# Performance work log

Measured on AMD Instinct MI355X. Metric: run time of the kernel, lower is better.

The kernel has to match this reference:

```python
import jax, jax.numpy as jnp
import numpy as np

ROPE_BASE = 10000.0

def _rope_tables(pos, d_head):
    # pos: (T,) int; returns cos,sin of shape (T, d_head//2)
    half = d_head // 2
    inv_freq = 1.0 / (ROPE_BASE ** (jnp.arange(half, dtype=jnp.float32) / half))
    ang = pos.astype(jnp.float32)[:, None] * inv_freq[None, :]
    return jnp.cos(ang), jnp.sin(ang)

def _apply_rope(x, cos, sin):
    # x: (B, H, T, D); cos/sin: (T, D//2); rotate-half convention
    x1, x2 = jnp.split(x, 2, axis=-1)
    c = cos[None, None, :, :]
    s = sin[None, None, :, :]
    return jnp.concatenate([x1 * c - x2 * s, x1 * s + x2 * c], axis=-1)

def setup_inputs() -> dict:
    key = jax.random.key(0)
    ks = jax.random.split(key, 8)
    B, T, C = 16, 4, 2048
    n_head, n_kv_head, d_head = 16, 4, 128
    S_cache = 4096
    sd = 1.0 / np.sqrt(C)
    return {
        "x": jax.random.normal(ks[0], (B, T, C), dtype=jnp.float32),
        "cache_k": jax.random.normal(ks[1], (B, n_kv_head, S_cache, d_head), dtype=jnp.float32),
        "cache_v": jax.random.normal(ks[2], (B, n_kv_head, S_cache, d_head), dtype=jnp.float32),
        "wq": jax.random.normal(ks[3], (C, n_head * d_head), dtype=jnp.float32) * sd,
        "wk": jax.random.normal(ks[4], (C, n_kv_head * d_head), dtype=jnp.float32) * sd,
        "wv": jax.random.normal(ks[5], (C, n_kv_head * d_head), dtype=jnp.float32) * sd,
        "w_proj": jax.random.normal(ks[6], (C, C), dtype=jnp.float32) * sd,
        "start_pos": 4096,
    }

def reference(x, cache_k, cache_v, wq, wk, wv, w_proj, start_pos):
    B, T, C = x.shape
    n_head, n_kv_head = 16, 4
    d_head = C // n_head
    group_size = n_head // n_kv_head
    sliding_window, sink = 2048, 4

    # projections -> (B, H, T, D)
    q = (x @ wq).reshape(B, T, n_head, d_head).transpose(0, 2, 1, 3)
    k = (x @ wk).reshape(B, T, n_kv_head, d_head).transpose(0, 2, 1, 3)
    v = (x @ wv).reshape(B, T, n_kv_head, d_head).transpose(0, 2, 1, 3)

    # RoPE at absolute positions [start_pos, start_pos+T)
    pos = jnp.arange(start_pos, start_pos + T)
    cos, sin = _rope_tables(pos, d_head)
    q = _apply_rope(q, cos, sin)
    k = _apply_rope(k, cos, sin)

    # KV cache concat along sequence dim
    k_all = jnp.concatenate([cache_k, k], axis=2)
    v_all = jnp.concatenate([cache_v, v], axis=2)

    # sliding window + attention sink slicing (4096+T > 2048+4)
    if k_all.shape[2] > sliding_window + sink:
        k_all = jnp.concatenate([k_all[:, :, :sink, :], k_all[:, :, -sliding_window:, :]], axis=2)
        v_all = jnp.concatenate([v_all[:, :, :sink, :], v_all[:, :, -sliding_window:, :]], axis=2)

    # GQA: expand KV heads to match query heads (repeat_interleave on head dim)
    k_attn = jnp.repeat(k_all, group_size, axis=1)
    v_attn = jnp.repeat(v_all, group_size, axis=1)

    # SDPA, is_causal=False (decode path with cache), dropout=0 (eval)
    scale = 1.0 / jnp.sqrt(jnp.float32(d_head))
    scores = jnp.einsum('bhtd,bhsd->bhts', q, k_attn) * scale
    attn = jax.nn.softmax(scores, axis=-1)
    y = jnp.einsum('bhts,bhsd->bhtd', attn, v_attn)

    y = y.transpose(0, 2, 1, 3).reshape(B, T, C)
    return y @ w_proj
```

## Files before the change

### kernel.cpp

```cpp
#include <hip/hip_runtime.h>
#include <math.h>

#define BB   16
#define TT   4
#define CC   2048
#define NH   16
#define NKV  4
#define DH   128
#define GRP  4
#define SCACHE 4096
#define SATT 2052
#define CS   128
#define NCH  17
#define KSPL 8

typedef unsigned int  uint32;
typedef unsigned short ushort_t;
typedef __attribute__((ext_vector_type(8))) __bf16 bf16x8;
typedef __attribute__((ext_vector_type(4))) float  f32x4;

__device__ __forceinline__ uint32 f2bf_bits(float f) {
    uint32 u = __float_as_uint(f);
    return (u + 0x7FFFu + ((u >> 16) & 1u)) >> 16;
}
__device__ __forceinline__ uint32 pk2(float lo, float hi) {
    return f2bf_bits(lo) | (f2bf_bits(hi) << 16);
}

#define Q_OFF    0
#define KNEW_OFF 524288
#define VNEW_OFF 655360
#define Y_OFF    786432
#define SCR_OFF  1310720

__global__ __launch_bounds__(256) void k_qkv(
    const float* __restrict__ x, const float* __restrict__ wq,
    const float* __restrict__ wk, const float* __restrict__ wv,
    float* __restrict__ part_qkv)
{
    __shared__ float xs[64][256];
    int ns = blockIdx.x, ks = blockIdx.y;
    int tid = threadIdx.x;
    int k0 = ks * 256;

    #pragma unroll
    for (int it = 0; it < 16; ++it) {
        int slot = it * 256 + tid;
        int row = slot >> 6, c4 = slot & 63;
        *(float4*)&xs[row][c4 * 4] = *(const float4*)(x + (size_t)row * CC + k0 + c4 * 4);
    }
    __syncthreads();

    int cp = tid & 31, rg = tid >> 5;
    const float* wp; int ldw, col;
    if (ns < 32)      { ldw = 2048; col = ns * 64 + cp * 2;
                        wp = wq + (size_t)k0 * 2048 + ns * 64 + cp * 2; }
    else if (ns < 40) { ldw = 512;  col = 2048 + (ns - 32) * 64 + cp * 2;
                        wp = wk + (size_t)k0 * 512 + (ns - 32) * 64 + cp * 2; }
    else              { ldw = 512;  col = 2560 + (ns - 40) * 64 + cp * 2;
                        wp = wv + (size_t)k0 * 512 + (ns - 40) * 64 + cp * 2; }

    float a[16];
    #pragma unroll
    for (int i = 0; i < 16; ++i) a[i] = 0.f;

    for (int k = 0; k < 256; k += 4) {
        float2 w0 = *(const float2*)(wp);
        float2 w1 = *(const float2*)(wp + ldw);
        float2 w2 = *(const float2*)(wp + 2 * ldw);
        float2 w3 = *(const float2*)(wp + 3 * ldw);
        wp += 4 * ldw;
        #pragma unroll
        for (int m = 0; m < 8; ++m) {
            float4 xv = *(const float4*)&xs[rg * 8 + m][k];
            float s0 = a[2*m], s1 = a[2*m+1];
            s0 = fmaf(xv.x, w0.x, s0); s1 = fmaf(xv.x, w0.y, s1);
            s0 = fmaf(xv.y, w1.x, s0); s1 = fmaf(xv.y, w1.y, s1);
            s0 = fmaf(xv.z, w2.x, s0); s1 = fmaf(xv.z, w2.y, s1);
            s0 = fmaf(xv.w, w3.x, s0); s1 = fmaf(xv.w, w3.y, s1);
            a[2*m] = s0; a[2*m+1] = s1;
        }
    }
    #pragma unroll
    for (int m = 0; m < 8; ++m)
        *(float2*)(part_qkv + ((size_t)(ks * 64 + rg * 8 + m) * 3072) + col) =
            make_float2(a[2*m], a[2*m+1]);
}

__global__ __launch_bounds__(256) void k_fix(
    const float* __restrict__ part_qkv, const int* __restrict__ spp,
    float* __restrict__ qws, float* __restrict__ knew, float* __restrict__ vnew)
{
    int u = blockIdx.x * 256 + threadIdx.x;
    int m = blockIdx.y;
    int b = m >> 2, t = m & 3;
    int sp = spp[0];
    const float NEG_L2_10K_64 = -0.20762050593048633f;

    if (u < 1024) {
        int h = u >> 6, d = u & 63;
        int col = h * 128 + d;
        float s1 = 0.f, s2 = 0.f;
        #pragma unroll
        for (int ks = 0; ks < KSPL; ++ks) {
            const float* p = part_qkv + (size_t)(ks * 64 + m) * 3072;
            s1 += p[col]; s2 += p[col + 64];
        }
        float inv = exp2f((float)d * NEG_L2_10K_64);
        float ang = (float)(sp + t) * inv;
        float cc = cosf(ang), ss = sinf(ang);
        float* dst = qws + (size_t)((b * NH + h) * TT + t) * DH + d;
        dst[0]  = s1 * cc - s2 * ss;
        dst[64] = s1 * ss + s2 * cc;
    } else if (u < 1280) {
        int v = u - 1024;
        int kv = v >> 6, d = v & 63;
        int col = 2048 + kv * 128 + d;
        float s1 = 0.f, s2 = 0.f;
        #pragma unroll
        for (int ks = 0; ks < KSPL; ++ks) {
            const float* p = part_qkv + (size_t)(ks * 64 + m) * 3072;
            s1 += p[col]; s2 += p[col + 64];
        }
        float inv = exp2f((float)d * NEG_L2_10K_64);
        float ang = (float)(sp + t) * inv;
        float cc = cosf(ang), ss = sinf(ang);
        float* dst = knew + (size_t)((b * NKV + kv) * TT + t) * DH + d;
        dst[0]  = s1 * cc - s2 * ss;
        dst[64] = s1 * ss + s2 * cc;
    } else {
        int v = u - 1280;
        int c0 = v * 2;
        int kv = c0 >> 7, dd = c0 & 127;
        float s1 = 0.f, s2 = 0.f;
        #pragma unroll
        for (int ks = 0; ks < KSPL; ++ks) {
            const float* p = part_qkv + (size_t)(ks * 64 + m) * 3072 + 2560 + c0;
            s1 += p[0]; s2 += p[1];
        }
        float* dst = vnew + (size_t)((b * NKV + kv) * TT + t) * DH + dd;
        dst[0] = s1; dst[1] = s2;
    }
}

__device__ __forceinline__ const float* kv_row(
    const float* cache, const float* newt, int bk, int j)
{
    if (j < 4)         return cache + ((size_t)bk * SCACHE + j) * DH;
    else if (j < 2048) return cache + ((size_t)bk * SCACHE + j + 2048) * DH;
    else               return newt  + ((size_t)(bk * TT + (j - 2048))) * DH;
}

__global__ __launch_bounds__(256) void k_attn(
    const float* __restrict__ qws,
    const float* __restrict__ kc, const float* __restrict__ vc,
    const float* __restrict__ knew, const float* __restrict__ vnew,
    float* __restrict__ part)
{
    __shared__ ushort_t vt_lds[128 * 136];
    __shared__ ushort_t p_lds[16 * 136];
    __shared__ float    red_a[64];
    __shared__ float    red_b[64];

    int bx = blockIdx.x;
    int c  = bx % NCH;
    int bk = bx / NCH;
    int b  = bk >> 2, kvh = bk & 3;
    int j0 = c * CS;
    int jn = (SATT - j0 < CS) ? (SATT - j0) : CS;
    int tid  = threadIdx.x;
    int wave = tid >> 6, lane = tid & 63;
    int quad = lane >> 4, l15 = lane & 15;
    const float scale = 0.08838834764831845f;

    int n0 = wave * 32;

    int rA = n0 + l15, rB = n0 + 16 + l15;
    const float* kA = kv_row(kc, knew, bk, j0 + (rA < jn ? rA : 0));
    const float* kB = kv_row(kc, knew, bk, j0 + (rB < jn ? rB : 0));
    float4 ka[8], kb[8];
    #pragma unroll
    for (int ks = 0; ks < 4; ++ks) {
        const float* pa = kA + ks * 32 + quad * 8;
        const float* pb = kB + ks * 32 + quad * 8;
        ka[2*ks]   = *(const float4*)pa;
        ka[2*ks+1] = *(const float4*)(pa + 4);
        kb[2*ks]   = *(const float4*)pb;
        kb[2*ks+1] = *(const float4*)(pb + 4);
    }

    int key0 = 2 * lane;
    bool okA = key0 < jn, okB = key0 + 1 < jn;
    const float* rva = kv_row(vc, vnew, bk, j0 + (okA ? key0 : 0));
    const float* rvb = kv_row(vc, vnew, bk, j0 + (okB ? key0 + 1 : 0));
    float4 va0[4], vb0[4];
    #pragma unroll
    for (int i = 0; i < 4; ++i) {
        int d = n0 + i * 4;
        va0[i] = *(const float4*)(rva + d);
        vb0[i] = *(const float4*)(rvb + d);
    }

    bf16x8 aq[4];
    {
        int h = kvh * GRP + (l15 >> 2), t = l15 & 3;
        const float* qr = qws + (size_t)((b * NH + h) * TT + t) * DH;
        #pragma unroll
        for (int ks = 0; ks < 4; ++ks) {
            const float* s = qr + ks * 32 + quad * 8;
            float4 f0 = *(const float4*)s;
            float4 f1 = *(const float4*)(s + 4);
            union { uint32 u[4]; bf16x8 v; } pk;
            pk.u[0] = pk2(f0.x, f0.y); pk.u[1] = pk2(f0.z, f0.w);
            pk.u[2] = pk2(f1.x, f1.y); pk.u[3] = pk2(f1.z, f1.w);
            aq[ks] = pk.v;
        }
    }

    f32x4 s0 = {0.f, 0.f, 0.f, 0.f}, s1 = {0.f, 0.f, 0.f, 0.f};
    #pragma unroll
    for (int ks = 0; ks < 4; ++ks) {
        union { uint32 u[4]; bf16x8 v; } pa, pb;
        pa.u[0] = pk2(ka[2*ks].x,   ka[2*ks].y);
        pa.u[1] = pk2(ka[2*ks].z,   ka[2*ks].w);
        pa.u[2] = pk2(ka[2*ks+1].x, ka[2*ks+1].y);
        pa.u[3] = pk2(ka[2*ks+1].z, ka[2*ks+1].w);
        pb.u[0] = pk2(kb[2*ks].x,   kb[2*ks].y);
        pb.u[1] = pk2(kb[2*ks].z,   kb[2*ks].w);
        pb.u[2] = pk2(kb[2*ks+1].x, kb[2*ks+1].y);
        pb.u[3] = pk2(kb[2*ks+1].z, kb[2*ks+1].w);
        s0 = __builtin_amdgcn_mfma_f32_16x16x32_bf16(aq[ks], pa.v, s0, 0, 0, 0);
        s1 = __builtin_amdgcn_mfma_f32_16x16x32_bf16(aq[ks], pb.v, s1, 0, 0, 0);
    }

    uint32* vt32 = (uint32*)vt_lds;
    #pragma unroll
    for (int i = 0; i < 4; ++i) {
        int d = n0 + i * 4;
        float4 fa = okA ? va0[i] : make_float4(0.f, 0.f, 0.f, 0.f);
        float4 fb = okB ? vb0[i] : make_float4(0.f, 0.f, 0.f, 0.f);
        vt32[(d + 0) * 68 + lane] = pk2(fa.x, fb.x);
        vt32[(d + 1) * 68 + lane] = pk2(fa.y, fb.y);
        vt32[(d + 2) * 68 + lane] = pk2(fa.z, fb.z);
        vt32[(d + 3) * 68 + lane] = pk2(fa.w, fb.w);
    }
    float4 va1[4], vb1[4];
    #pragma unroll
    for (int i = 0; i < 4; ++i) {
        int d = n0 + 16 + i * 4;
        va1[i] = *(const float4*)(rva + d);
        vb1[i] = *(const float4*)(rvb + d);
    }

    int c0 = n0 + l15, c1 = n0 + 16 + l15;
    bool v0ok = c0 < jn, v1ok = c1 < jn;
    float sc0[4], sc1[4];
    #pragma unroll
    for (int i = 0; i < 4; ++i) {
        sc0[i] = v0ok ? s0[i] * scale : -1e30f;
        sc1[i] = v1ok ? s1[i] * scale : -1e30f;
        float v = fmaxf(sc0[i], sc1[i]);
        v = fmaxf(v, __shfl_xor(v, 1));
        v = fmaxf(v, __shfl_xor(v, 2));
        v = fmaxf(v, __shfl_xor(v, 4));
        v = fmaxf(v, __shfl_xor(v, 8));
        if (l15 == 0) red_a[wave * 16 + quad * 4 + i] = v;
    }
    __syncthreads();

    #pragma unroll
    for (int i = 0; i < 4; ++i) {
        int r = quad * 4 + i;
        float M = fmaxf(fmaxf(red_a[r], red_a[16 + r]),
                        fmaxf(red_a[32 + r], red_a[48 + r]));
        float p0 = __expf(sc0[i] - M);
        float p1 = __expf(sc1[i] - M);
        p_lds[r * 136 + c0] = (ushort_t)f2bf_bits(p0);
        p_lds[r * 136 + c1] = (ushort_t)f2bf_bits(p1);
        float v = p0 + p1;
        v += __shfl_xor(v, 1);
        v += __shfl_xor(v, 2);
        v += __shfl_xor(v, 4);
        v += __shfl_xor(v, 8);
        if (l15 == 0) red_b[wave * 16 + r] = v;
    }

    #pragma unroll
    for (int i = 0; i < 4; ++i) {
        int d = n0 + 16 + i * 4;
        float4 fa = okA ? va1[i] : make_float4(0.f, 0.f, 0.f, 0.f);
        float4 fb = okB ? vb1[i] : make_float4(0.f, 0.f, 0.f, 0.f);
        vt32[(d + 0) * 68 + lane] = pk2(fa.x, fb.x);
        vt32[(d + 1) * 68 + lane] = pk2(fa.y, fb.y);
        vt32[(d + 2) * 68 + lane] = pk2(fa.z, fb.z);
        vt32[(d + 3) * 68 + lane] = pk2(fa.w, fb.w);
    }
    __syncthreads();

    if (tid < 16) {
        int r = tid;
        float M = fmaxf(fmaxf(red_a[r], red_a[16 + r]),
                        fmaxf(red_a[32 + r], red_a[48 + r]));
        float L = red_b[r] + red_b[16 + r] + red_b[32 + r] + red_b[48 + r];
        float* rp = part + ((size_t)(bk * NCH + c) * 16 + r) * 132;
        rp[0] = M; rp[1] = L;
    }

    int d0 = wave * 32;
    f32x4 o0 = {0.f, 0.f, 0.f, 0.f}, o1 = {0.f, 0.f, 0.f, 0.f};
    #pragma unroll
    for (int ks = 0; ks < 4; ++ks) {
        bf16x8 ap = *(const bf16x8*)&p_lds[l15 * 136 + ks * 32 + quad * 8];
        bf16x8 b0 = *(const bf16x8*)&vt_lds[(d0 + l15) * 136 + ks * 32 + quad * 8];
        bf16x8 b1 = *(const bf16x8*)&vt_lds[(d0 + 16 + l15) * 136 + ks * 32 + quad * 8];
        o0 = __builtin_amdgcn_mfma_f32_16x16x32_bf16(ap, b0, o0, 0, 0, 0);
        o1 = __builtin_amdgcn_mfma_f32_16x16x32_bf16(ap, b1, o1, 0, 0, 0);
    }
    float* dstb = part + (size_t)(bk * NCH + c) * 16 * 132;
    #pragma unroll
    for (int i = 0; i < 4; ++i) {
        int row = quad * 4 + i;
        dstb[row * 132 + 4 + d0 + l15]      = o0[i];
        dstb[row * 132 + 4 + d0 + 16 + l15] = o1[i];
    }
}

__global__ __launch_bounds__(128) void k_comb(
    const float* __restrict__ part, float* __restrict__ yws)
{
    int bx = blockIdx.x;
    int t = bx & 3, h = (bx >> 2) & 15, b = bx >> 6;
    int bk = b * NKV + (h >> 2);
    int r  = (h & 3) * 4 + t;
    int d  = threadIdx.x;
    float M = -1e30f;
    for (int c = 0; c < NCH; ++c)
        M = fmaxf(M, part[((size_t)(bk * NCH + c) * 16 + r) * 132]);
    float L = 0.f, y = 0.f;
    for (int c = 0; c < NCH; ++c) {
        const float* pp = part + ((size_t)(bk * NCH + c) * 16 + r) * 132;
        float w = __expf(pp[0] - M);
        L += w * pp[1];
        y  = fmaf(w, pp[4 + d], y);
    }
    yws[(size_t)(b * TT + t) * CC + h * DH + d] = y / L;
}

__global__ __launch_bounds__(256) void k_proj(
    const float* __restrict__ yws, const float* __restrict__ wp,
    float* __restrict__ part_p)
{
    __shared__ float xs[64][256];
    int ns = blockIdx.x, ks = blockIdx.y;
    int tid = threadIdx.x;
    int k0 = ks * 256;
    #pragma unroll
    for (int it = 0; it < 16; ++it) {
        int slot = it * 256 + tid;
        int row = slot >> 6, c4 = slot & 63;
        *(float4*)&xs[row][c4 * 4] = *(const float4*)(yws + (size_t)row * CC + k0 + c4 * 4);
    }
    __syncthreads();

    int cp = tid & 31, rg = tid >> 5;
    int n = ns * 64 + cp * 2;
    const float* w = wp + (size_t)k0 * CC + n;
    float a[16];
    #pragma unroll
    for (int i = 0; i < 16; ++i) a[i] = 0.f;

    for (int k = 0; k < 256; k += 4) {
        float2 w0 = *(const float2*)(w);
        float2 w1 = *(const float2*)(w + CC);
        float2 w2 = *(const float2*)(w + 2 * CC);
        float2 w3 = *(const float2*)(w + 3 * CC);
        w += 4 * CC;
        #pragma unroll
        for (int m = 0; m < 8; ++m) {
            float4 xv = *(const float4*)&xs[rg * 8 + m][k];
            float s0 = a[2*m], s1 = a[2*m+1];
            s0 = fmaf(xv.x, w0.x, s0); s1 = fmaf(xv.x, w0.y, s1);
            s0 = fmaf(xv.y, w1.x, s0); s1 = fmaf(xv.y, w1.y, s1);
            s0 = fmaf(xv.z, w2.x, s0); s1 = fmaf(xv.z, w2.y, s1);
            s0 = fmaf(xv.w, w3.x, s0); s1 = fmaf(xv.w, w3.y, s1);
            a[2*m] = s0; a[2*m+1] = s1;
        }
    }
    #pragma unroll
    for (int m = 0; m < 8; ++m)
        *(float2*)(part_p + ((size_t)(ks * 64 + rg * 8 + m) * CC) + n) =
            make_float2(a[2*m], a[2*m+1]);
}

__global__ __launch_bounds__(256) void k_out(
    const float* __restrict__ part_p, float* __restrict__ out)
{
    int gt = blockIdx.x * 256 + threadIdx.x;
    float s = 0.f;
    #pragma unroll
    for (int ks = 0; ks < KSPL; ++ks) s += part_p[(size_t)ks * 64 * CC + gt];
    out[gt] = s;
}

extern "C" void kernel_launch(void* const* d_in, const int* in_sizes, int n_in,
                              void* d_out, int out_size, void* d_ws, size_t ws_size,
                              hipStream_t stream)
{
    const float* x   = (const float*)d_in[0];
    const float* ck  = (const float*)d_in[1];
    const float* cv  = (const float*)d_in[2];
    const float* wq  = (const float*)d_in[3];
    const float* wk  = (const float*)d_in[4];
    const float* wv  = (const float*)d_in[5];
    const float* wpj = (const float*)d_in[6];
    const int*   sp  = (const int*)d_in[7];
    char* ws = (char*)d_ws;
    float* qws  = (float*)(ws + Q_OFF);
    float* knew = (float*)(ws + KNEW_OFF);
    float* vnew = (float*)(ws + VNEW_OFF);
    float* yws  = (float*)(ws + Y_OFF);
    float* scr  = (float*)(ws + SCR_OFF);
    float* out  = (float*)d_out;

    hipLaunchKernelGGL(k_qkv,  dim3(48, 8),   dim3(256), 0, stream, x, wq, wk, wv, scr);
    hipLaunchKernelGGL(k_fix,  dim3(6, 64),   dim3(256), 0, stream, scr, sp, qws, knew, vnew);
    hipLaunchKernelGGL(k_attn, dim3(64 * NCH), dim3(256), 0, stream, qws, ck, cv, knew, vnew, scr);
    hipLaunchKernelGGL(k_comb, dim3(1024),    dim3(128), 0, stream, scr, yws);
    hipLaunchKernelGGL(k_proj, dim3(32, 8),   dim3(256), 0, stream, yws, wpj, scr);
    hipLaunchKernelGGL(k_out,  dim3(512),     dim3(256), 0, stream, scr, out);
}
```

Measured before the change: 369.0 us.

## Make attention chunk waves independent with per-wave softmax and cross-wave merge

Each wave now owns 32 keys: it computes a local max and exp, writes its own P and a transposed, XOR-swizzled bf16 V tile into private LDS, and runs the full P·V over all 128 head dims. The block-wide max barrier between QK and PV goes away. Partial outputs from the four waves are rescaled and summed through LDS at the end, and the softmax scale is folded into Q before the bf16 conversion. This trades an extra LDS reduction pass and more accumulator registers for less synchronisation and fewer bank conflicts.

```diff
diff --git a/kernel.cpp b/kernel.cpp
--- a/kernel.cpp
+++ b/kernel.cpp
@@ -26,6 +26,7 @@
 __device__ __forceinline__ uint32 pk2(float lo, float hi) {
     return f2bf_bits(lo) | (f2bf_bits(hi) << 16);
 }
+#define F4C(v, j) ((j)==0 ? (v).x : (j)==1 ? (v).y : (j)==2 ? (v).z : (v).w)
 
 #define Q_OFF    0
 #define KNEW_OFF 524288
@@ -157,10 +158,7 @@
     const float* __restrict__ knew, const float* __restrict__ vnew,
     float* __restrict__ part)
 {
-    __shared__ ushort_t vt_lds[128 * 136];
-    __shared__ ushort_t p_lds[16 * 136];
-    __shared__ float    red_a[64];
-    __shared__ float    red_b[64];
+    __shared__ __align__(16) uint32 smem[9600];
 
     int bx = blockIdx.x;
     int c  = bx % NCH;
@@ -169,36 +167,39 @@
     int j0 = c * CS;
     int jn = (SATT - j0 < CS) ? (SATT - j0) : CS;
     int tid  = threadIdx.x;
-    int wave = tid >> 6, lane = tid & 63;
+    int w    = tid >> 6, lane = tid & 63;
     int quad = lane >> 4, l15 = lane & 15;
     const float scale = 0.08838834764831845f;
 
-    int n0 = wave * 32;
-
-    int rA = n0 + l15, rB = n0 + 16 + l15;
-    const float* kA = kv_row(kc, knew, bk, j0 + (rA < jn ? rA : 0));
-    const float* kB = kv_row(kc, knew, bk, j0 + (rB < jn ? rB : 0));
+    uint32*   vt    = smem + w * 2048;
+    ushort_t* pl    = (ushort_t*)(smem + 8448) + w * 512;
+    float*    red_m = (float*)(smem + 9472);
+    float*    red_l = red_m + 64;
+    float*    o_all = (float*)smem;
+
+    int base = w * 32;
+
+    int rA = base + l15, rB = base + 16 + l15;
+    const float* kAp = kv_row(kc, knew, bk, j0 + (rA < jn ? rA : 0));
+    const float* kBp = kv_row(kc, knew, bk, j0 + (rB < jn ? rB : 0));
     float4 ka[8], kb[8];
     #pragma unroll
     for (int ks = 0; ks < 4; ++ks) {
-        const float* pa = kA + ks * 32 + quad * 8;
-        const float* pb = kB + ks * 32 + quad * 8;
-        ka[2*ks]   = *(const float4*)pa;
-        ka[2*ks+1] = *(const float4*)(pa + 4);
-        kb[2*ks]   = *(const float4*)pb;
-        kb[2*ks+1] = *(const float4*)(pb + 4);
-    }
-
-    int key0 = 2 * lane;
-    bool okA = key0 < jn, okB = key0 + 1 < jn;
+        ka[2*ks]   = *(const float4*)(kAp + ks * 32 + quad * 8);
+        ka[2*ks+1] = *(const float4*)(kAp + ks * 32 + quad * 8 + 4);
+        kb[2*ks]   = *(const float4*)(kBp + ks * 32 + quad * 8);
+        kb[2*ks+1] = *(const float4*)(kBp + ks * 32 + quad * 8 + 4);
+    }
+
+    int key0 = base + 2 * l15, key1 = key0 + 1;
+    bool okA = key0 < jn, okB = key1 < jn;
     const float* rva = kv_row(vc, vnew, bk, j0 + (okA ? key0 : 0));
-    const float* rvb = kv_row(vc, vnew, bk, j0 + (okB ? key0 + 1 : 0));
-    float4 va0[4], vb0[4];
-    #pragma unroll
-    for (int i = 0; i < 4; ++i) {
-        int d = n0 + i * 4;
-        va0[i] = *(const float4*)(rva + d);
-        vb0[i] = *(const float4*)(rvb + d);
+    const float* rvb = kv_row(vc, vnew, bk, j0 + (okB ? key1 : 0));
+    float4 va[4], vb[4];
+    #pragma unroll
+    for (int i = 0; i < 4; ++i) {
+        va[i] = *(const float4*)(rva + quad * 32 + i * 4);
+        vb[i] = *(const float4*)(rvb + quad * 32 + i * 4);
     }
 
     bf16x8 aq[4];
@@ -207,13 +208,14 @@
         const float* qr = qws + (size_t)((b * NH + h) * TT + t) * DH;
         #pragma unroll
         for (int ks = 0; ks < 4; ++ks) {
-            const float* s = qr + ks * 32 + quad * 8;
-            float4 f0 = *(const float4*)s;
-            float4 f1 = *(const float4*)(s + 4);
-            union { uint32 u[4]; bf16x8 v; } pk;
-            pk.u[0] = pk2(f0.x, f0.y); pk.u[1] = pk2(f0.z, f0.w);
-            pk.u[2] = pk2(f1.x, f1.y); pk.u[3] = pk2(f1.z, f1.w);
-            aq[ks] = pk.v;
+            float4 f0 = *(const float4*)(qr + ks * 32 + quad * 8);
+            float4 f1 = *(const float4*)(qr + ks * 32 + quad * 8 + 4);
+            union { uint32 u[4]; bf16x8 v; } pk_;
+            pk_.u[0] = pk2(f0.x * scale, f0.y * scale);
+            pk_.u[1] = pk2(f0.z * scale, f0.w * scale);
+            pk_.u[2] = pk2(f1.x * scale, f1.y * scale);
+            pk_.u[3] = pk2(f1.z * scale, f1.w * scale);
+            aq[ks] = pk_.v;
         }
     }
 
@@ -233,95 +235,113 @@
         s1 = __builtin_amdgcn_mfma_f32_16x16x32_bf16(aq[ks], pb.v, s1, 0, 0, 0);
     }
 
-    uint32* vt32 = (uint32*)vt_lds;
-    #pragma unroll
-    for (int i = 0; i < 4; ++i) {
-        int d = n0 + i * 4;
-        float4 fa = okA ? va0[i] : make_float4(0.f, 0.f, 0.f, 0.f);
-        float4 fb = okB ? vb0[i] : make_float4(0.f, 0.f, 0.f, 0.f);
-        vt32[(d + 0) * 68 + lane] = pk2(fa.x, fb.x);
-        vt32[(d + 1) * 68 + lane] = pk2(fa.y, fb.y);
-        vt32[(d + 2) * 68 + lane] = pk2(fa.z, fb.z);
-        vt32[(d + 3) * 68 + lane] = pk2(fa.w, fb.w);
-    }
-    float4 va1[4], vb1[4];
-    #pragma unroll
-    for (int i = 0; i < 4; ++i) {
-        int d = n0 + 16 + i * 4;
-        va1[i] = *(const float4*)(rva + d);
-        vb1[i] = *(const float4*)(rvb + d);
-    }
-
-    int c0 = n0 + l15, c1 = n0 + 16 + l15;
-    bool v0ok = c0 < jn, v1ok = c1 < jn;
-    float sc0[4], sc1[4];
-    #pragma unroll
-    for (int i = 0; i < 4; ++i) {
-        sc0[i] = v0ok ? s0[i] * scale : -1e30f;
-        sc1[i] = v1ok ? s1[i] * scale : -1e30f;
+    #pragma unroll
+    for (int i = 0; i < 4; ++i) {
+        #pragma unroll
+        for (int jj = 0; jj < 4; ++jj) {
+            int dd = i * 4 + jj;
+            int d  = quad * 32 + dd;
+            int sw = (dd ^ (dd >> 2)) & 3;
+            float fa = okA ? F4C(va[i], jj) : 0.f;
+            float fb = okB ? F4C(vb[i], jj) : 0.f;
+            vt[d * 16 + ((((l15 >> 2) ^ sw) << 2) | (l15 & 3))] = pk2(fa, fb);
+        }
+    }
+    float4 va2[4], vb2[4];
+    #pragma unroll
+    for (int i = 0; i < 4; ++i) {
+        va2[i] = *(const float4*)(rva + quad * 32 + 16 + i * 4);
+        vb2[i] = *(const float4*)(rvb + quad * 32 + 16 + i * 4);
+    }
+
+    bool c0ok = (base + l15) < jn, c1ok = (base + 16 + l15) < jn;
+    float sc0[4], sc1[4], mloc[4];
+    #pragma unroll
+    for (int i = 0; i < 4; ++i) {
+        sc0[i] = c0ok ? s0[i] : -1e30f;
+        sc1[i] = c1ok ? s1[i] : -1e30f;
         float v = fmaxf(sc0[i], sc1[i]);
         v = fmaxf(v, __shfl_xor(v, 1));
         v = fmaxf(v, __shfl_xor(v, 2));
         v = fmaxf(v, __shfl_xor(v, 4));
         v = fmaxf(v, __shfl_xor(v, 8));
-        if (l15 == 0) red_a[wave * 16 + quad * 4 + i] = v;
-    }
+        mloc[i] = v;
+        float p0 = __expf(sc0[i] - v);
+        float p1 = __expf(sc1[i] - v);
+        int r   = quad * 4 + i;
+        int swr = (i ^ quad) & 3;
+        pl[r * 32 + ((((l15 >> 3)    ) ^ swr) << 3) + (l15 & 7)] = (ushort_t)f2bf_bits(p0);
+        pl[r * 32 + ((((l15 >> 3) | 2) ^ swr) << 3) + (l15 & 7)] = (ushort_t)f2bf_bits(p1);
+        float su = p0 + p1;
+        su += __shfl_xor(su, 1);
+        su += __shfl_xor(su, 2);
+        su += __shfl_xor(su, 4);
+        su += __shfl_xor(su, 8);
+        if (l15 == 0) { red_m[w * 16 + r] = v; red_l[w * 16 + r] = su; }
+    }
+
+    #pragma unroll
+    for (int i = 0; i < 4; ++i) {
+        #pragma unroll
+        for (int jj = 0; jj < 4; ++jj) {
+            int dd = 16 + i * 4 + jj;
+            int d  = quad * 32 + dd;
+            int sw = (dd ^ (dd >> 2)) & 3;
+            float fa = okA ? F4C(va2[i], jj) : 0.f;
+            float fb = okB ? F4C(vb2[i], jj) : 0.f;
+            vt[d * 16 + ((((l15 >> 2) ^ sw) << 2) | (l15 & 3))] = pk2(fa, fb);
+        }
+    }
+
+    int swp = (l15 ^ (l15 >> 2)) & 3;
+    bf16x8 ap = *(const bf16x8*)&pl[l15 * 32 + ((quad ^ swp) << 3)];
+    f32x4 o[8];
+    #pragma unroll
+    for (int t = 0; t < 8; ++t) o[t] = (f32x4){0.f, 0.f, 0.f, 0.f};
+    #pragma unroll
+    for (int t = 0; t < 8; ++t) {
+        int d   = t * 16 + l15;
+        int swv = (d ^ (d >> 2)) & 3;
+        bf16x8 bv = *(const bf16x8*)&vt[d * 16 + ((quad ^ swv) << 2)];
+        o[t] = __builtin_amdgcn_mfma_f32_16x16x32_bf16(ap, bv, o[t], 0, 0, 0);
+    }
+
     __syncthreads();
-
     #pragma unroll
     for (int i = 0; i < 4; ++i) {
         int r = quad * 4 + i;
-        float M = fmaxf(fmaxf(red_a[r], red_a[16 + r]),
-                        fmaxf(red_a[32 + r], red_a[48 + r]));
-        float p0 = __expf(sc0[i] - M);
-        float p1 = __expf(sc1[i] - M);
-        p_lds[r * 136 + c0] = (ushort_t)f2bf_bits(p0);
-        p_lds[r * 136 + c1] = (ushort_t)f2bf_bits(p1);
-        float v = p0 + p1;
-        v += __shfl_xor(v, 1);
-        v += __shfl_xor(v, 2);
-        v += __shfl_xor(v, 4);
-        v += __shfl_xor(v, 8);
-        if (l15 == 0) red_b[wave * 16 + r] = v;
-    }
-
-    #pragma unroll
-    for (int i = 0; i < 4; ++i) {
-        int d = n0 + 16 + i * 4;
-        float4 fa = okA ? va1[i] : make_float4(0.f, 0.f, 0.f, 0.f);
-        float4 fb = okB ? vb1[i] : make_float4(0.f, 0.f, 0.f, 0.f);
-        vt32[(d + 0) * 68 + lane] = pk2(fa.x, fb.x);
-        vt32[(d + 1) * 68 + lane] = pk2(fa.y, fb.y);
-        vt32[(d + 2) * 68 + lane] = pk2(fa.z, fb.z);
-        vt32[(d + 3) * 68 + lane] = pk2(fa.w, fb.w);
+        float Mb = fmaxf(fmaxf(red_m[r], red_m[16 + r]),
+                         fmaxf(red_m[32 + r], red_m[48 + r]));
+        float scl = __expf(mloc[i] - Mb);
+        #pragma unroll
+        for (int t = 0; t < 8; ++t)
+            o_all[(w * 16 + r) * 132 + t * 16 + l15] = o[t][i] * scl;
     }
     __syncthreads();
-
-    if (tid < 16) {
-        int r = tid;
-        float M = fmaxf(fmaxf(red_a[r], red_a[16 + r]),
-                        fmaxf(red_a[32 + r], red_a[48 + r]));
-        float L = red_b[r] + red_b[16 + r] + red_b[32 + r] + red_b[48 + r];
-        float* rp = part + ((size_t)(bk * NCH + c) * 16 + r) * 132;
-        rp[0] = M; rp[1] = L;
-    }
-
-    int d0 = wave * 32;
-    f32x4 o0 = {0.f, 0.f, 0.f, 0.f}, o1 = {0.f, 0.f, 0.f, 0.f};
-    #pragma unroll
-    for (int ks = 0; ks < 4; ++ks) {
-        bf16x8 ap = *(const bf16x8*)&p_lds[l15 * 136 + ks * 32 + quad * 8];
-        bf16x8 b0 = *(const bf16x8*)&vt_lds[(d0 + l15) * 136 + ks * 32 + quad * 8];
-        bf16x8 b1 = *(const bf16x8*)&vt_lds[(d0 + 16 + l15) * 136 + ks * 32 + quad * 8];
-        o0 = __builtin_amdgcn_mfma_f32_16x16x32_bf16(ap, b0, o0, 0, 0, 0);
-        o1 = __builtin_amdgcn_mfma_f32_16x16x32_bf16(ap, b1, o1, 0, 0, 0);
-    }
-    float* dstb = part + (size_t)(bk * NCH + c) * 16 * 132;
-    #pragma unroll
-    for (int i = 0; i < 4; ++i) {
-        int row = quad * 4 + i;
-        dstb[row * 132 + 4 + d0 + l15]      = o0[i];
-        dstb[row * 132 + 4 + d0 + 16 + l15] = o1[i];
+    {
+        int r = tid >> 4, dg = tid & 15;
+        float acc[8];
+        #pragma unroll
+        for (int jj = 0; jj < 8; ++jj) acc[jj] = 0.f;
+        #pragma unroll
+        for (int ww = 0; ww < 4; ++ww) {
+            const float* src = &o_all[(ww * 16 + r) * 132 + dg * 8];
+            #pragma unroll
+            for (int jj = 0; jj < 8; ++jj) acc[jj] += src[jj];
+        }
+        float* dstb = part + (size_t)(bk * NCH + c) * 16 * 132;
+        #pragma unroll
+        for (int jj = 0; jj < 8; ++jj) dstb[r * 132 + 4 + dg * 8 + jj] = acc[jj];
+        if (dg == 0) {
+            float Mb = fmaxf(fmaxf(red_m[r], red_m[16 + r]),
+                             fmaxf(red_m[32 + r], red_m[48 + r]));
+            float L = 0.f;
+            #pragma unroll
+            for (int ww = 0; ww < 4; ++ww)
+                L += __expf(red_m[ww * 16 + r] - Mb) * red_l[ww * 16 + r];
+            dstb[r * 132 + 0] = Mb;
+            dstb[r * 132 + 1] = L;
+        }
     }
 }
 
```

New measurement: 368.3 us. Within noise of the previous version (-0.2%).
